# Kernel optimization log

Hardware: AMD Instinct MI355X
Metric: run time of the kernel (lower is better)

Reference implementation:

```python
import jax, jax.numpy as jnp
import numpy as np
from jax import lax

B, T, I, H = 4096, 64, 8, 128


def _lstm_layer(xs, W_ih, W_hh, b):
    # xs: [T, B, D_in]; PyTorch gate order i, f, g, o
    def step(carry, x_t):
        h, c = carry
        gates = x_t @ W_ih.T + h @ W_hh.T + b  # [B, 4H]
        i, f, g, o = jnp.split(gates, 4, axis=-1)
        i = jax.nn.sigmoid(i)
        f = jax.nn.sigmoid(f)
        g = jnp.tanh(g)
        o = jax.nn.sigmoid(o)
        c_new = f * c + i * g
        h_new = o * jnp.tanh(c_new)
        return (h_new, c_new), h_new

    n_b = xs.shape[1]
    h0 = jnp.zeros((n_b, W_hh.shape[1]), xs.dtype)
    c0 = jnp.zeros((n_b, W_hh.shape[1]), xs.dtype)
    (h_last, _), ys = lax.scan(step, (h0, c0), xs)
    return ys, h_last


def setup_inputs() -> dict:
    key = jax.random.key(0)
    ks = jax.random.split(key, 14)
    s = 1.0 / np.sqrt(H)
    u = lambda k, shape: jax.random.uniform(k, shape, jnp.float32, -s, s)
    return {
        "x": jax.random.normal(ks[0], (B, T, I), jnp.float32),
        "W_ih0": u(ks[1], (4 * H, I)),
        "W_hh0": u(ks[2], (4 * H, H)),
        "b_ih0": u(ks[3], (4 * H,)),
        "b_hh0": u(ks[4], (4 * H,)),
        "W_ih1": u(ks[5], (4 * H, H)),
        "W_hh1": u(ks[6], (4 * H, H)),
        "b_ih1": u(ks[7], (4 * H,)),
        "b_hh1": u(ks[8], (4 * H,)),
        "W_d1": u(ks[9], (5, H)),
        "b_d1": u(ks[10], (5,)),
        "W_d2": u(ks[11], (1, 5)),
        "b_d2": u(ks[12], (1,)),
    }


def reference(x, W_ih0, W_hh0, b_ih0, b_hh0, W_ih1, W_hh1, b_ih1, b_hh1,
              W_d1, b_d1, W_d2, b_d2):
    xs = jnp.transpose(x, (1, 0, 2))  # [T, B, I]
    ys0, _ = _lstm_layer(xs, W_ih0, W_hh0, b_ih0 + b_hh0)
    # inter-layer dropout (p=0.2) and trailing Dropout are identity in eval mode
    _, h_last = _lstm_layer(ys0, W_ih1, W_hh1, b_ih1 + b_hh1)  # [B, H]
    out = jax.nn.relu(h_last)
    out = jax.nn.relu(out @ W_d1.T + b_d1)  # [B, 5]
    out = out @ W_d2.T + b_d2  # [B, 1]
    return out
```

## Files before the change

kernel.cpp:

```cpp
#include <hip/hip_runtime.h>

typedef _Float16 h8 __attribute__((ext_vector_type(8)));
typedef _Float16 h4 __attribute__((ext_vector_type(4)));
typedef float f4 __attribute__((ext_vector_type(4)));

#define B_ 4096
#define T_ 64
#define I_ 8
#define H_ 128

#define WC0_OFF 0
#define H0_OFF  131072
#define H1_OFF  139264
#define LDS_TOTAL 147456

#define LOG2E    1.4426950408889634f
#define TWOLOG2E 2.8853900817779268f

__device__ __forceinline__ float sigm2_(float v) {
    return __builtin_amdgcn_rcpf(1.f + exp2f(-v));
}
__device__ __forceinline__ float tanh2_(float v) {
    return 1.f - 2.f * __builtin_amdgcn_rcpf(exp2f(v) + 1.f);
}
__device__ __forceinline__ float tanhn_(float v) {
    return 1.f - 2.f * __builtin_amdgcn_rcpf(exp2f(TWOLOG2E * v) + 1.f);
}

__global__ __launch_bounds__(512, 1) void lstm_fused_kernel(
    const float* __restrict__ x,
    const float* __restrict__ Wih0, const float* __restrict__ Whh0,
    const float* __restrict__ bih0, const float* __restrict__ bhh0,
    const float* __restrict__ Wih1, const float* __restrict__ Whh1,
    const float* __restrict__ bih1, const float* __restrict__ bhh1,
    const float* __restrict__ Wd1, const float* __restrict__ bd1,
    const float* __restrict__ Wd2, const float* __restrict__ bd2,
    float* __restrict__ out)
{
    __shared__ __align__(16) unsigned char lds[LDS_TOTAL];
    const int tid = threadIdx.x;
    const int w   = tid >> 6;
    const int l   = tid & 63;
    const int c16 = l & 15;
    const int G4  = l >> 4;
    const int rowbase = blockIdx.x * 16;
    const int swzl = (l & 7) << 4;

    {
        const int p  = tid;
        const int q  = p & 3;
        const int gs = q * H_ + (p >> 6) * 16 + ((p >> 2) & 3) * 4 + ((p >> 4) & 3);
        const float sc = (q == 2) ? TWOLOG2E : LOG2E;
        const float* src = Whh0 + (size_t)gs * H_;
        const int swz = (p & 7) << 4;
        unsigned char* dst = lds + WC0_OFF + p * 256;
#pragma unroll
        for (int kb = 0; kb < 16; kb++) {
            float4 f0 = *(const float4*)(src + kb * 8);
            float4 f1 = *(const float4*)(src + kb * 8 + 4);
            h8 v;
            v[0]=(_Float16)(f0.x*sc); v[1]=(_Float16)(f0.y*sc);
            v[2]=(_Float16)(f0.z*sc); v[3]=(_Float16)(f0.w*sc);
            v[4]=(_Float16)(f1.x*sc); v[5]=(_Float16)(f1.y*sc);
            v[6]=(_Float16)(f1.z*sc); v[7]=(_Float16)(f1.w*sc);
            *(h8*)(dst + ((kb * 16) ^ swz)) = v;
        }
    }
    {
        f4 z = {0.f, 0.f, 0.f, 0.f};
        if (tid < 256) *(f4*)(lds + H0_OFF + 4096 + tid * 16) = z;
        else           *(f4*)(lds + H1_OFF + 4096 + (tid - 256) * 16) = z;
    }

    h8 wc1[4][8];
    h4 ax16[4];
    f4 b1[4];
    {
        const int rq = c16 & 3;
        const float sc1 = (rq == 2) ? TWOLOG2E : LOG2E;
#pragma unroll
        for (int j = 0; j < 4; j++) {
            const int gs = rq * H_ + w * 16 + (c16 >> 2) * 4 + j;
#pragma unroll
            for (int ks = 0; ks < 8; ks++) {
                const int k0 = ks * 32 + G4 * 8;
                const float* src = (k0 < 128) ? (Whh1 + (size_t)gs * H_ + k0)
                                              : (Wih1 + (size_t)gs * H_ + (k0 - 128));
                float4 f0 = *(const float4*)src;
                float4 f1 = *(const float4*)(src + 4);
                h8 v;
                v[0]=(_Float16)(f0.x*sc1); v[1]=(_Float16)(f0.y*sc1);
                v[2]=(_Float16)(f0.z*sc1); v[3]=(_Float16)(f0.w*sc1);
                v[4]=(_Float16)(f1.x*sc1); v[5]=(_Float16)(f1.y*sc1);
                v[6]=(_Float16)(f1.z*sc1); v[7]=(_Float16)(f1.w*sc1);
                wc1[j][ks] = v;
            }
            h4 a;
#pragma unroll
            for (int e = 0; e < 4; e++) {
                const int k = G4 * 4 + e;
                float val = 0.f;
                if (k < 8)       val = Wih0[(size_t)gs * I_ + k] * sc1;
                else if (k == 8) val = (bih0[gs] + bhh0[gs]) * sc1;
                a[e] = (_Float16)val;
            }
            ax16[j] = a;
            f4 bb;
#pragma unroll
            for (int q2 = 0; q2 < 4; q2++) {
                const int gs2 = q2 * H_ + w * 16 + G4 * 4 + j;
                bb[q2] = (bih1[gs2] + bhh1[gs2]) * ((q2 == 2) ? TWOLOG2E : LOG2E);
            }
            b1[j] = bb;
        }
    }

    const float* xrow = x + (size_t)(rowbase + c16) * T_ * I_;
    float4 xf0 = *(const float4*)(xrow);
    float4 xf1 = *(const float4*)(xrow + 4);

    float c0r[4] = {0.f, 0.f, 0.f, 0.f};
    float c1r[4] = {0.f, 0.f, 0.f, 0.f};

    __syncthreads();

    int cur = 0;
    for (int t = 0; t < T_; t++) {
        h4 bx;
        bx[0] = (_Float16)0.f; bx[1] = (_Float16)0.f;
        bx[2] = (_Float16)0.f; bx[3] = (_Float16)0.f;
        if (G4 == 0) {
            bx[0]=(_Float16)xf0.x; bx[1]=(_Float16)xf0.y;
            bx[2]=(_Float16)xf0.z; bx[3]=(_Float16)xf0.w;
        } else if (G4 == 1) {
            bx[0]=(_Float16)xf1.x; bx[1]=(_Float16)xf1.y;
            bx[2]=(_Float16)xf1.z; bx[3]=(_Float16)xf1.w;
        } else if (G4 == 2) {
            bx[0] = (_Float16)1.f;
        }
        if (t < T_ - 1) {
            xf0 = *(const float4*)(xrow + (t + 1) * 8);
            xf1 = *(const float4*)(xrow + (t + 1) * 8 + 4);
        }

        f4 acc0[4], acc1[4];
        {
            f4 z = {0.f, 0.f, 0.f, 0.f};
#pragma unroll
            for (int j = 0; j < 4; j++) acc0[j] = z;
        }
        const unsigned char* h0rd = lds + H0_OFF + (cur ^ 1) * 4096;
#pragma unroll
        for (int ks = 0; ks < 4; ks++) {
            h8 b = *(const h8*)(h0rd + ((c16 * 256 + ks * 64 + G4 * 16) ^ swzl));
#pragma unroll
            for (int j = 0; j < 4; j++) {
                h8 a = *(const h8*)(lds + WC0_OFF + (w * 64 + j * 16 + c16) * 256
                                    + ((ks * 64 + G4 * 16) ^ swzl));
                acc0[j] = __builtin_amdgcn_mfma_f32_16x16x32_f16(a, b, acc0[j], 0, 0, 0);
            }
        }
#pragma unroll
        for (int j = 0; j < 4; j++)
            acc0[j] = __builtin_amdgcn_mfma_f32_16x16x16f16(ax16[j], bx, acc0[j], 0, 0, 0);

        const unsigned char* h1rd = lds + H1_OFF + (cur ^ 1) * 4096;
#pragma unroll
        for (int j = 0; j < 4; j++) acc1[j] = b1[j];
#pragma unroll
        for (int ks = 0; ks < 4; ks++) {
            h8 b = *(const h8*)(h1rd + ((c16 * 256 + ks * 64 + G4 * 16) ^ swzl));
#pragma unroll
            for (int j = 0; j < 4; j++)
                acc1[j] = __builtin_amdgcn_mfma_f32_16x16x32_f16(wc1[j][ks], b, acc1[j], 0, 0, 0);
        }

        unsigned char* h0wr = lds + H0_OFF + cur * 4096;
        {
            h4 hv;
#pragma unroll
            for (int j = 0; j < 4; j++) {
                const float vi = sigm2_(acc0[j][0]);
                const float vf = sigm2_(acc0[j][1]);
                const float vg = tanh2_(acc0[j][2]);
                const float vo = sigm2_(acc0[j][3]);
                const float cn = vf * c0r[j] + vi * vg;
                c0r[j] = cn;
                hv[j] = (_Float16)(vo * tanhn_(cn));
            }
            *(h4*)(h0wr + ((c16 * 256 + w * 32 + G4 * 8) ^ swzl)) = hv;
        }

        __syncthreads();

        const unsigned char* h0n = lds + H0_OFF + cur * 4096;
#pragma unroll
        for (int ks = 0; ks < 4; ks++) {
            h8 b = *(const h8*)(h0n + ((c16 * 256 + ks * 64 + G4 * 16) ^ swzl));
#pragma unroll
            for (int j = 0; j < 4; j++)
                acc1[j] = __builtin_amdgcn_mfma_f32_16x16x32_f16(wc1[j][ks + 4], b, acc1[j], 0, 0, 0);
        }
        unsigned char* h1wr = lds + H1_OFF + cur * 4096;
        {
            h4 hv;
#pragma unroll
            for (int j = 0; j < 4; j++) {
                const float vi = sigm2_(acc1[j][0]);
                const float vf = sigm2_(acc1[j][1]);
                const float vg = tanh2_(acc1[j][2]);
                const float vo = sigm2_(acc1[j][3]);
                const float cn = vf * c1r[j] + vi * vg;
                c1r[j] = cn;
                hv[j] = (_Float16)(vo * tanhn_(cn));
            }
            *(h4*)(h1wr + ((c16 * 256 + w * 32 + G4 * 8) ^ swzl)) = hv;
        }

        __syncthreads();
        cur ^= 1;
    }

    if (tid < 128) {
        const int r = tid >> 3, part = tid & 7;
        const unsigned char* h1f = lds + H1_OFF + 4096;
        const int rswz = (r & 7) << 4;
        float s0 = 0.f, s1 = 0.f, s2 = 0.f, s3 = 0.f, s4 = 0.f;
#pragma unroll
        for (int kk = 0; kk < 16; kk++) {
            const int k = part * 16 + kk;
            float a = (float)*(const _Float16*)(h1f + ((r * 256 + k * 2) ^ rswz));
            a = fmaxf(a, 0.f);
            s0 += a * Wd1[0 * H_ + k];
            s1 += a * Wd1[1 * H_ + k];
            s2 += a * Wd1[2 * H_ + k];
            s3 += a * Wd1[3 * H_ + k];
            s4 += a * Wd1[4 * H_ + k];
        }
#pragma unroll
        for (int m = 1; m < 8; m <<= 1) {
            s0 += __shfl_xor(s0, m);
            s1 += __shfl_xor(s1, m);
            s2 += __shfl_xor(s2, m);
            s3 += __shfl_xor(s3, m);
            s4 += __shfl_xor(s4, m);
        }
        if (part == 0) {
            float o = bd2[0];
            o += fmaxf(s0 + bd1[0], 0.f) * Wd2[0];
            o += fmaxf(s1 + bd1[1], 0.f) * Wd2[1];
            o += fmaxf(s2 + bd1[2], 0.f) * Wd2[2];
            o += fmaxf(s3 + bd1[3], 0.f) * Wd2[3];
            o += fmaxf(s4 + bd1[4], 0.f) * Wd2[4];
            out[rowbase + r] = o;
        }
    }
}

extern "C" void kernel_launch(void* const* d_in, const int* in_sizes, int n_in,
                              void* d_out, int out_size, void* d_ws, size_t ws_size,
                              hipStream_t stream)
{
    const float* x    = (const float*)d_in[0];
    const float* Wih0 = (const float*)d_in[1];
    const float* Whh0 = (const float*)d_in[2];
    const float* bih0 = (const float*)d_in[3];
    const float* bhh0 = (const float*)d_in[4];
    const float* Wih1 = (const float*)d_in[5];
    const float* Whh1 = (const float*)d_in[6];
    const float* bih1 = (const float*)d_in[7];
    const float* bhh1 = (const float*)d_in[8];
    const float* Wd1  = (const float*)d_in[9];
    const float* bd1  = (const float*)d_in[10];
    const float* Wd2  = (const float*)d_in[11];
    const float* bd2  = (const float*)d_in[12];

    lstm_fused_kernel<<<B_ / 16, 512, 0, stream>>>(
        x, Wih0, Whh0, bih0, bhh0, Wih1, Whh1, bih1, bhh1,
        Wd1, bd1, Wd2, bd2, (float*)d_out);
}
```

Baseline: 209.7 us.

## Keep layer-1 weights in AGPRs via inline-asm MFMA and move biases to LDS

```diff
diff --git a/kernel.cpp b/kernel.cpp
--- a/kernel.cpp
+++ b/kernel.cpp
@@ -3,6 +3,7 @@
 typedef _Float16 h8 __attribute__((ext_vector_type(8)));
 typedef _Float16 h4 __attribute__((ext_vector_type(4)));
 typedef float f4 __attribute__((ext_vector_type(4)));
+typedef int i4v __attribute__((ext_vector_type(4)));
 
 #define B_ 4096
 #define T_ 64
@@ -12,7 +13,8 @@
 #define WC0_OFF 0
 #define H0_OFF  131072
 #define H1_OFF  139264
-#define LDS_TOTAL 147456
+#define BB_OFF  147456
+#define LDS_TOTAL 149504
 
 #define LOG2E    1.4426950408889634f
 #define TWOLOG2E 2.8853900817779268f
@@ -26,8 +28,29 @@
 __device__ __forceinline__ float tanhn_(float v) {
     return 1.f - 2.f * __builtin_amdgcn_rcpf(exp2f(TWOLOG2E * v) + 1.f);
 }
-
-__global__ __launch_bounds__(512, 1) void lstm_fused_kernel(
+__device__ __forceinline__ int gs_of(int p) {
+    return (p & 3) * H_ + (p >> 6) * 16 + ((p >> 2) & 3) * 4 + ((p >> 4) & 3);
+}
+__device__ __forceinline__ float scl_(int q) { return (q == 2) ? TWOLOG2E : LOG2E; }
+
+__device__ __forceinline__ void mfma_v(f4& acc, const h8& a, const h8& b) {
+    asm volatile("v_mfma_f32_16x16x32_f16 %0, %1, %2, %0"
+                 : "+v"(acc) : "v"(a), "v"(b));
+}
+__device__ __forceinline__ void mfma_v0(f4& acc, const h8& a, const h8& b) {
+    asm volatile("s_nop 2\n\tv_mfma_f32_16x16x32_f16 %0, %1, %2, %0"
+                 : "+v"(acc) : "v"(a), "v"(b));
+}
+__device__ __forceinline__ void mfma_a(f4& acc, const i4v& a, const h8& b) {
+    asm volatile("v_mfma_f32_16x16x32_f16 %0, %1, %2, %0"
+                 : "+v"(acc) : "a"(a), "v"(b));
+}
+__device__ __forceinline__ void mfma_a_last(f4& acc, const i4v& a, const h8& b) {
+    asm volatile("v_mfma_f32_16x16x32_f16 %0, %1, %2, %0\n\ts_nop 7\n\ts_nop 7"
+                 : "+v"(acc) : "a"(a), "v"(b));
+}
+
+__global__ void lstm_fused_kernel(
     const float* __restrict__ x,
     const float* __restrict__ Wih0, const float* __restrict__ Whh0,
     const float* __restrict__ bih0, const float* __restrict__ bhh0,
@@ -48,9 +71,8 @@
 
     {
         const int p  = tid;
-        const int q  = p & 3;
-        const int gs = q * H_ + (p >> 6) * 16 + ((p >> 2) & 3) * 4 + ((p >> 4) & 3);
-        const float sc = (q == 2) ? TWOLOG2E : LOG2E;
+        const int gs = gs_of(p);
+        const float sc = scl_(p & 3);
         const float* src = Whh0 + (size_t)gs * H_;
         const int swz = (p & 7) << 4;
         unsigned char* dst = lds + WC0_OFF + p * 256;
@@ -70,17 +92,17 @@
         f4 z = {0.f, 0.f, 0.f, 0.f};
         if (tid < 256) *(f4*)(lds + H0_OFF + 4096 + tid * 16) = z;
         else           *(f4*)(lds + H1_OFF + 4096 + (tid - 256) * 16) = z;
-    }
-
-    h8 wc1[4][8];
+        const int gs = gs_of(tid);
+        ((float*)(lds + BB_OFF))[tid] = (bih1[gs] + bhh1[gs]) * scl_(tid & 3);
+    }
+
+    i4v wc1a[4][8];
     h4 ax16[4];
-    f4 b1[4];
     {
-        const int rq = c16 & 3;
-        const float sc1 = (rq == 2) ? TWOLOG2E : LOG2E;
+        const float sc1 = scl_(c16 & 3);
 #pragma unroll
         for (int j = 0; j < 4; j++) {
-            const int gs = rq * H_ + w * 16 + (c16 >> 2) * 4 + j;
+            const int gs = gs_of(w * 64 + j * 16 + c16);
 #pragma unroll
             for (int ks = 0; ks < 8; ks++) {
                 const int k0 = ks * 32 + G4 * 8;
@@ -93,7 +115,7 @@
                 v[2]=(_Float16)(f0.z*sc1); v[3]=(_Float16)(f0.w*sc1);
                 v[4]=(_Float16)(f1.x*sc1); v[5]=(_Float16)(f1.y*sc1);
                 v[6]=(_Float16)(f1.z*sc1); v[7]=(_Float16)(f1.w*sc1);
-                wc1[j][ks] = v;
+                wc1a[j][ks] = *(i4v*)&v;
             }
             h4 a;
 #pragma unroll
@@ -105,15 +127,13 @@
                 a[e] = (_Float16)val;
             }
             ax16[j] = a;
-            f4 bb;
-#pragma unroll
-            for (int q2 = 0; q2 < 4; q2++) {
-                const int gs2 = q2 * H_ + w * 16 + G4 * 4 + j;
-                bb[q2] = (bih1[gs2] + bhh1[gs2]) * ((q2 == 2) ? TWOLOG2E : LOG2E);
-            }
-            b1[j] = bb;
-        }
-    }
+        }
+    }
+#pragma unroll
+    for (int j = 0; j < 4; j++)
+#pragma unroll
+        for (int ks = 0; ks < 8; ks++)
+            asm volatile("" : "+a"(wc1a[j][ks]));
 
     const float* xrow = x + (size_t)(rowbase + c16) * T_ * I_;
     float4 xf0 = *(const float4*)(xrow);
@@ -157,7 +177,8 @@
             for (int j = 0; j < 4; j++) {
                 h8 a = *(const h8*)(lds + WC0_OFF + (w * 64 + j * 16 + c16) * 256
                                     + ((ks * 64 + G4 * 16) ^ swzl));
-                acc0[j] = __builtin_amdgcn_mfma_f32_16x16x32_f16(a, b, acc0[j], 0, 0, 0);
+                if (ks == 0) mfma_v0(acc0[j], a, b);
+                else         mfma_v(acc0[j], a, b);
             }
         }
 #pragma unroll
@@ -166,13 +187,14 @@
 
         const unsigned char* h1rd = lds + H1_OFF + (cur ^ 1) * 4096;
 #pragma unroll
-        for (int j = 0; j < 4; j++) acc1[j] = b1[j];
+        for (int j = 0; j < 4; j++)
+            acc1[j] = *(const f4*)(lds + BB_OFF + (w * 64 + j * 16 + G4 * 4) * 4);
 #pragma unroll
         for (int ks = 0; ks < 4; ks++) {
             h8 b = *(const h8*)(h1rd + ((c16 * 256 + ks * 64 + G4 * 16) ^ swzl));
 #pragma unroll
             for (int j = 0; j < 4; j++)
-                acc1[j] = __builtin_amdgcn_mfma_f32_16x16x32_f16(wc1[j][ks], b, acc1[j], 0, 0, 0);
+                mfma_a(acc1[j], wc1a[j][ks], b);
         }
 
         unsigned char* h0wr = lds + H0_OFF + cur * 4096;
@@ -198,8 +220,10 @@
         for (int ks = 0; ks < 4; ks++) {
             h8 b = *(const h8*)(h0n + ((c16 * 256 + ks * 64 + G4 * 16) ^ swzl));
 #pragma unroll
-            for (int j = 0; j < 4; j++)
-                acc1[j] = __builtin_amdgcn_mfma_f32_16x16x32_f16(wc1[j][ks + 4], b, acc1[j], 0, 0, 0);
+            for (int j = 0; j < 4; j++) {
+                if (ks == 3 && j == 3) mfma_a_last(acc1[j], wc1a[j][ks + 4], b);
+                else                   mfma_a(acc1[j], wc1a[j][ks + 4], b);
+            }
         }
         unsigned char* h1wr = lds + H1_OFF + cur * 4096;
         {
```

After: 731.8 us. +249.0%, slower.
